# Optimization experiments

Measured on AMD Instinct MI355X. Metric: run time of the kernel, lower is better.

Reference implementation:

```python
import jax, jax.numpy as jnp
import numpy as np

H = 16         # num query heads
KV = 8         # num kv heads
HD = 64        # head_dim
WINDOW = 512   # sliding window size
ROPE_BASE = 10000.0


def rotate_half(x):
    x1, x2 = x[..., : x.shape[-1] // 2], x[..., x.shape[-1] // 2 :]
    return jnp.concatenate((-x2, x1), axis=-1)


def rope_cos_sin(seq_len, dim, dtype):
    inv_freq = 1.0 / (ROPE_BASE ** (jnp.arange(0, dim, 2, dtype=jnp.float32) / dim))
    t = jnp.arange(seq_len, dtype=jnp.float32)
    freqs = jnp.outer(t, inv_freq)              # [S, dim/2]
    emb = jnp.concatenate((freqs, freqs), axis=-1)  # [S, dim]
    return jnp.cos(emb).astype(dtype), jnp.sin(emb).astype(dtype)


def setup_inputs() -> dict:
    key = jax.random.key(0)
    ks = jax.random.split(key, 5)
    B, S, D = 2, 2048, 1024
    std = 0.02
    return {
        "hidden_states": jax.random.normal(ks[0], (B, S, D), dtype=jnp.float32),
        "Wq": jax.random.normal(ks[1], (D, H * HD), dtype=jnp.float32) * std,
        "Wk": jax.random.normal(ks[2], (D, KV * HD), dtype=jnp.float32) * std,
        "Wv": jax.random.normal(ks[3], (D, KV * HD), dtype=jnp.float32) * std,
        "Wo": jax.random.normal(ks[4], (H * HD, D), dtype=jnp.float32) * std,
    }


def reference(hidden_states, Wq, Wk, Wv, Wo):
    B, S, D = hidden_states.shape
    n_rep = H // KV

    q = (hidden_states @ Wq).reshape(B, S, H, HD).transpose(0, 2, 1, 3)   # [B,H,S,hd]
    k = (hidden_states @ Wk).reshape(B, S, KV, HD).transpose(0, 2, 1, 3)  # [B,KV,S,hd]
    v = (hidden_states @ Wv).reshape(B, S, KV, HD).transpose(0, 2, 1, 3)

    cos, sin = rope_cos_sin(S, HD, q.dtype)  # [S,hd]
    cos = cos[None, None]
    sin = sin[None, None]
    q = q * cos + rotate_half(q) * sin
    k = k * cos + rotate_half(k) * sin

    # repeat kv heads for GQA ([:, :, None] expand + reshape == repeat along head axis)
    k = jnp.repeat(k, n_rep, axis=1)  # [B,H,S,hd]
    v = jnp.repeat(v, n_rep, axis=1)

    scores = jnp.einsum("bhqd,bhkd->bhqk", q, k) / jnp.sqrt(jnp.asarray(HD, q.dtype))
    i = jnp.arange(S)[:, None]
    j = jnp.arange(S)[None, :]
    allowed = (j <= i) & (j >= i - WINDOW)  # causal + sliding window
    scores = jnp.where(allowed[None, None], scores, -jnp.inf)

    attn = jax.nn.softmax(scores, axis=-1)
    out = jnp.einsum("bhqk,bhkd->bhqd", attn, v)          # [B,H,S,hd]
    out = out.transpose(0, 2, 1, 3).reshape(B, S, H * HD)  # [B,S,D]
    return out @ Wo
```

## Files before the change

kernel.cpp:

```cpp
#include <hip/hip_runtime.h>
#include <hip/hip_bf16.h>

typedef __attribute__((ext_vector_type(8))) short short8;
typedef __attribute__((ext_vector_type(4))) float f32x4;

#define S_LEN 2048
#define NH 16
#define NKV 8
#define HD 64
#define WIN 512
#define DMODEL 1024
#define LOG2_10000 13.287712379549449f

#define GLOAD16(g, l)                                                        \
    __builtin_amdgcn_global_load_lds(                                        \
        (const __attribute__((address_space(1))) unsigned int*)(g),          \
        (__attribute__((address_space(3))) unsigned int*)(l), 16, 0, 0)

__device__ __forceinline__ int xcd_swz(int lin, int nwg) {
    return (lin & 7) * (nwg >> 3) + (lin >> 3);
}

__global__ void prep_kernel(const float* __restrict__ X,
                            const float* __restrict__ W0,
                            const float* __restrict__ W1,
                            const float* __restrict__ W2,
                            const float* __restrict__ W3,
                            __hip_bfloat16* __restrict__ Xb,
                            __hip_bfloat16* __restrict__ WqkvT,
                            __hip_bfloat16* __restrict__ WoT) {
    if (blockIdx.z == 4) {
        int tid = (blockIdx.y * 32 + blockIdx.x) * 256 + threadIdx.y * 32 + threadIdx.x;
        const float4* Xi = reinterpret_cast<const float4*>(X);
#pragma unroll
        for (int r = 0; r < 4; ++r) {
            int i = tid + r * (1024 * 256);
            float4 v = Xi[i];
            alignas(8) __hip_bfloat16 h[4];
            h[0] = __float2bfloat16(v.x);
            h[1] = __float2bfloat16(v.y);
            h[2] = __float2bfloat16(v.z);
            h[3] = __float2bfloat16(v.w);
            *reinterpret_cast<ushort4*>(Xb + (size_t)i * 4) =
                *reinterpret_cast<ushort4*>(h);
        }
        return;
    }
    __shared__ float tile[32][33];
    const int K = DMODEL;
    const float* W;
    __hip_bfloat16* WT;
    int N;
    switch (blockIdx.z) {
        case 0: W = W0; WT = WqkvT;                          N = 1024; break;
        case 1: W = W1; WT = WqkvT + (size_t)1024 * K;       N = 512;  break;
        case 2: W = W2; WT = WqkvT + (size_t)1536 * K;       N = 512;  break;
        default: W = W3; WT = WoT;                           N = 1024; break;
    }
    if ((int)blockIdx.x * 32 >= N) return;
    int nx = blockIdx.x * 32 + threadIdx.x;
    int k0 = blockIdx.y * 32;
#pragma unroll
    for (int r = 0; r < 4; ++r) {
        int k = k0 + threadIdx.y + r * 8;
        tile[threadIdx.y + r * 8][threadIdx.x] = W[(size_t)k * N + nx];
    }
    __syncthreads();
#pragma unroll
    for (int r = 0; r < 4; ++r) {
        int nn = blockIdx.x * 32 + threadIdx.y + r * 8;
        int kk = k0 + threadIdx.x;
        WT[(size_t)nn * K + kk] = __float2bfloat16(tile[threadIdx.x][threadIdx.y + r * 8]);
    }
}

__global__ __launch_bounds__(256, 2) void gemm_qkv_kernel(
    const __hip_bfloat16* __restrict__ A,
    const __hip_bfloat16* __restrict__ BT,
    __hip_bfloat16* __restrict__ Qo,
    __hip_bfloat16* __restrict__ Ko,
    __hip_bfloat16* __restrict__ VTo) {
    const int K = DMODEL;
    __shared__ __hip_bfloat16 ldsA[2][128 * 64];
    __shared__ __hip_bfloat16 ldsB[2][128 * 64];
    const int tx = threadIdx.x;
    const int wave = tx >> 6;
    const int lane = tx & 63;
    const int l16 = lane & 15;
    const int quad = lane >> 4;
    const int swz = xcd_swz(blockIdx.x + 16 * blockIdx.y, 512);
    const int col0 = (swz & 15) * 128;
    const int row0 = (swz >> 4) * 128;
    const int wrow = (wave >> 1) * 64;
    const int wcol = (wave & 1) * 64;
    const int sw = l16 & 7;

    f32x4 acc[4][4] = {};

    const int arow = tx >> 3;
    const int cs8 = ((tx & 7) ^ (arow & 7)) * 8;
    const __hip_bfloat16* gA = A + (size_t)(row0 + arow) * K + cs8;
    const __hip_bfloat16* gB = BT + (size_t)(col0 + arow) * K + cs8;

    auto stage = [&](int k0, int bf) {
        char* lA = (char*)(&ldsA[bf][0]) + tx * 16;
        char* lB = (char*)(&ldsB[bf][0]) + tx * 16;
#pragma unroll
        for (int r = 0; r < 4; ++r) {
            GLOAD16(gA + (size_t)(r * 32) * K + k0, lA + r * 4096);
            GLOAD16(gB + (size_t)(r * 32) * K + k0, lB + r * 4096);
        }
    };

    stage(0, 0);
    int buf = 0;
    for (int k0 = 0; k0 < K; k0 += 64) {
        __syncthreads();
        if (k0 + 64 < K) stage(k0 + 64, buf ^ 1);
        short8 af[4][2], bf4[4][2];
#pragma unroll
        for (int i = 0; i < 4; ++i) {
            const char* ar = (const char*)(&ldsA[buf][0]) + (wrow + i * 16 + l16) * 128;
            const char* br = (const char*)(&ldsB[buf][0]) + (wcol + i * 16 + l16) * 128;
#pragma unroll
            for (int ks = 0; ks < 2; ++ks) {
                af[i][ks] = *reinterpret_cast<const short8*>(
                    ar + (((ks * 4 + quad) ^ sw) << 4));
                bf4[i][ks] = *reinterpret_cast<const short8*>(
                    br + (((ks * 4 + quad) ^ sw) << 4));
            }
        }
#pragma unroll
        for (int ks = 0; ks < 2; ++ks)
#pragma unroll
            for (int mi = 0; mi < 4; ++mi)
#pragma unroll
                for (int ni = 0; ni < 4; ++ni)
                    acc[mi][ni] = __builtin_amdgcn_mfma_f32_16x16x32_bf16(
                        af[mi][ks], bf4[ni][ks], acc[mi][ni], 0, 0, 0);
        buf ^= 1;
    }

    const int rbase = row0 + wrow;
    const int cbaseg = col0 + wcol;
    const bool isQ = (cbaseg < DMODEL);
    const bool isK = (cbaseg >= DMODEL) && (cbaseg < DMODEL + 512);
    if (isQ || isK) {
        float invf[2];
        invf[0] = exp2f(-(float)(l16)      * (LOG2_10000 / 32.0f));
        invf[1] = exp2f(-(float)(16 + l16) * (LOG2_10000 / 32.0f));
#pragma unroll
        for (int mi = 0; mi < 4; ++mi)
#pragma unroll
            for (int r = 0; r < 4; ++r) {
                int srow = (rbase + mi * 16 + quad * 4 + r) & (S_LEN - 1);
#pragma unroll
                for (int ni = 0; ni < 2; ++ni) {
                    float ang = (float)srow * invf[ni];
                    float c = __cosf(ang), s = __sinf(ang);
                    float x1 = acc[mi][ni][r], x2 = acc[mi][ni + 2][r];
                    acc[mi][ni][r]     = x1 * c - x2 * s;
                    acc[mi][ni + 2][r] = x2 * c + x1 * s;
                }
            }
        __hip_bfloat16* Co = isQ ? Qo : Ko;
        int cbase = isQ ? cbaseg : cbaseg - DMODEL;
        int rowstride = isQ ? (NH * HD) : (NKV * HD);
#pragma unroll
        for (int mi = 0; mi < 4; ++mi)
#pragma unroll
            for (int ni = 0; ni < 4; ++ni) {
                size_t col = cbase + ni * 16 + l16;
#pragma unroll
                for (int r = 0; r < 4; ++r)
                    Co[(size_t)(rbase + mi * 16 + quad * 4 + r) * rowstride + col] =
                        __float2bfloat16(acc[mi][ni][r]);
            }
    } else {
        int bb = row0 >> 11;
#pragma unroll
        for (int mi = 0; mi < 4; ++mi) {
            int s = ((rbase + mi * 16 + quad * 4) & (S_LEN - 1));
#pragma unroll
            for (int ni = 0; ni < 4; ++ni) {
                int colv = cbaseg - 1536 + ni * 16 + l16;
                int vh = colv >> 6, d = colv & 63;
                alignas(8) __hip_bfloat16 hv[4];
#pragma unroll
                for (int r = 0; r < 4; ++r) hv[r] = __float2bfloat16(acc[mi][ni][r]);
                *reinterpret_cast<ushort4*>(
                    VTo + ((size_t)(bb * NKV + vh) * HD + d) * S_LEN + s) =
                    *reinterpret_cast<ushort4*>(hv);
            }
        }
    }
}

__global__ __launch_bounds__(256, 4) void gemm_op_kernel(
    const __hip_bfloat16* __restrict__ A,
    const __hip_bfloat16* __restrict__ BT,
    float* __restrict__ Co, int N, int K) {
    __shared__ __hip_bfloat16 ldsA[2][128 * 64];
    __shared__ __hip_bfloat16 ldsB[2][64 * 64];
    const int tx = threadIdx.x;
    const int wave = tx >> 6;
    const int lane = tx & 63;
    const int l16 = lane & 15;
    const int quad = lane >> 4;
    const int swz = xcd_swz(blockIdx.x + 16 * blockIdx.y, 512);
    const int col0 = (swz & 15) * 64;
    const int row0 = (swz >> 4) * 128;
    const int wrow = wave * 32;
    const int sw = l16 & 7;

    f32x4 acc[2][4] = {};

    const int arow = tx >> 3;
    const int cs8 = ((tx & 7) ^ (arow & 7)) * 8;
    const __hip_bfloat16* gA = A + (size_t)(row0 + arow) * K + cs8;
    const __hip_bfloat16* gB = BT + (size_t)(col0 + arow) * K + cs8;

    auto stage = [&](int k0, int bf) {
        char* lA = (char*)(&ldsA[bf][0]) + tx * 16;
        char* lB = (char*)(&ldsB[bf][0]) + tx * 16;
#pragma unroll
        for (int r = 0; r < 4; ++r)
            GLOAD16(gA + (size_t)(r * 32) * K + k0, lA + r * 4096);
#pragma unroll
        for (int r = 0; r < 2; ++r)
            GLOAD16(gB + (size_t)(r * 32) * K + k0, lB + r * 4096);
    };

    stage(0, 0);
    int buf = 0;
    for (int k0 = 0; k0 < K; k0 += 64) {
        __syncthreads();
        if (k0 + 64 < K) stage(k0 + 64, buf ^ 1);
        short8 af[2][2], bf4[4][2];
#pragma unroll
        for (int i = 0; i < 2; ++i) {
            const char* ar = (const char*)(&ldsA[buf][0]) + (wrow + i * 16 + l16) * 128;
#pragma unroll
            for (int ks = 0; ks < 2; ++ks)
                af[i][ks] = *reinterpret_cast<const short8*>(
                    ar + (((ks * 4 + quad) ^ sw) << 4));
        }
#pragma unroll
        for (int i = 0; i < 4; ++i) {
            const char* br = (const char*)(&ldsB[buf][0]) + (i * 16 + l16) * 128;
#pragma unroll
            for (int ks = 0; ks < 2; ++ks)
                bf4[i][ks] = *reinterpret_cast<const short8*>(
                    br + (((ks * 4 + quad) ^ sw) << 4));
        }
#pragma unroll
        for (int ks = 0; ks < 2; ++ks)
#pragma unroll
            for (int mi = 0; mi < 2; ++mi)
#pragma unroll
                for (int ni = 0; ni < 4; ++ni)
                    acc[mi][ni] = __builtin_amdgcn_mfma_f32_16x16x32_bf16(
                        af[mi][ks], bf4[ni][ks], acc[mi][ni], 0, 0, 0);
        buf ^= 1;
    }

    const int rbase = row0 + wrow;
#pragma unroll
    for (int mi = 0; mi < 2; ++mi)
#pragma unroll
        for (int ni = 0; ni < 4; ++ni) {
            size_t col = col0 + ni * 16 + l16;
#pragma unroll
            for (int r = 0; r < 4; ++r)
                Co[(size_t)(rbase + mi * 16 + quad * 4 + r) * N + col] = acc[mi][ni][r];
        }
}

__global__ __launch_bounds__(256, 4) void attn_mfma_kernel(
    const __hip_bfloat16* __restrict__ Q,
    const __hip_bfloat16* __restrict__ K,
    const __hip_bfloat16* __restrict__ VT,
    __hip_bfloat16* __restrict__ O) {
    __shared__ __hip_bfloat16 ldsK[2][64][64];
    __shared__ __hip_bfloat16 ldsVT[2][64][64];
    __shared__ __hip_bfloat16 ldsP[4][16][64];
    const int tx = threadIdx.x;
    const int wave = tx >> 6;
    const int lane = tx & 63;
    const int l16 = lane & 15;
    const int quad = lane >> 4;
    const int swz = xcd_swz(blockIdx.x + 32 * (blockIdx.y + 16 * blockIdx.z), 1024);
    const int q0 = (swz & 31) * 64;
    const int h = (swz >> 5) & 15;
    const int b = swz >> 9;
    const int kvh = h >> 1;
    const int qi = q0 + wave * 16 + l16;

    short8 aq[2];
    {
        const __hip_bfloat16* qp =
            Q + (size_t)(b * S_LEN + qi) * (NH * HD) + h * HD + quad * 8;
        aq[0] = *reinterpret_cast<const short8*>(qp);
        aq[1] = *reinterpret_cast<const short8*>(qp + 32);
    }
    f32x4 acc_o[4] = {};
    float m = -1e30f, l = 0.f;
    const float SL2 = 0.125f * 1.4426950408889634f;

    const int s_row = tx >> 3;
    const int s_c8 = (((tx & 7) ^ (s_row & 7))) * 8;
    const int sw = (l16 & 7);
    auto stage = [&](int j0, int bf) {
        char* lk = (char*)(&ldsK[bf][0][0]) + tx * 16;
        char* lv = (char*)(&ldsVT[bf][0][0]) + tx * 16;
#pragma unroll
        for (int r = 0; r < 2; ++r) {
            int row = s_row + r * 32;
            GLOAD16(K + (size_t)(b * S_LEN + j0 + row) * (NKV * HD) + kvh * HD + s_c8,
                    lk + r * 4096);
            GLOAD16(VT + ((size_t)(b * NKV + kvh) * HD + row) * S_LEN + j0 + s_c8,
                    lv + r * 4096);
        }
    };

    const int kstart = (q0 >= WIN) ? (q0 - WIN) : 0;
    stage(kstart, 0);
    int buf = 0;

    char* prow = (char*)(&ldsP[wave][l16][0]);

    for (int j0 = kstart; j0 <= q0; j0 += 64) {
        __syncthreads();
        if (j0 + 64 <= q0) stage(j0 + 64, buf ^ 1);

        f32x4 sacc[4] = {};
#pragma unroll
        for (int t = 0; t < 4; ++t) {
            const __hip_bfloat16* krow = &ldsK[buf][t * 16 + l16][0];
            short8 bk0 = *reinterpret_cast<const short8*>(krow + ((quad ^ sw) * 8));
            short8 bk1 = *reinterpret_cast<const short8*>(krow + (((4 + quad) ^ sw) * 8));
            sacc[t] = __builtin_amdgcn_mfma_f32_16x16x32_bf16(bk0, aq[0], sacc[t], 0, 0, 0);
            sacc[t] = __builtin_amdgcn_mfma_f32_16x16x32_bf16(bk1, aq[1], sacc[t], 0, 0, 0);
        }

        const bool need_mask = (j0 == q0) || (q0 >= WIN && j0 == kstart);
        float sv[4][4];
        if (need_mask) {
#pragma unroll
            for (int t = 0; t < 4; ++t)
#pragma unroll
                for (int r = 0; r < 4; ++r) {
                    int j = j0 + t * 16 + quad * 4 + r;
                    bool ok = (j <= qi) && (j + WIN >= qi);
                    sv[t][r] = ok ? sacc[t][r] * SL2 : -1e30f;
                }
        } else {
#pragma unroll
            for (int t = 0; t < 4; ++t)
#pragma unroll
                for (int r = 0; r < 4; ++r) sv[t][r] = sacc[t][r] * SL2;
        }
        float cm = -1e30f;
#pragma unroll
        for (int t = 0; t < 4; ++t)
#pragma unroll
            for (int r = 0; r < 4; ++r) cm = fmaxf(cm, sv[t][r]);
        cm = fmaxf(cm, __shfl_xor(cm, 16));
        cm = fmaxf(cm, __shfl_xor(cm, 32));
        if (!__all(cm - m <= 8.0f)) {
            float mn = fmaxf(m, cm);
            float alpha = exp2f(m - mn);
            m = mn;
            l *= alpha;
#pragma unroll
            for (int t = 0; t < 4; ++t)
#pragma unroll
                for (int r = 0; r < 4; ++r) acc_o[t][r] *= alpha;
        }
        float sp = 0.f;
#pragma unroll
        for (int t = 0; t < 4; ++t)
#pragma unroll
            for (int r = 0; r < 4; ++r) { sv[t][r] = exp2f(sv[t][r] - m); sp += sv[t][r]; }
        sp += __shfl_xor(sp, 16);
        sp += __shfl_xor(sp, 32);
        l += sp;
#pragma unroll
        for (int t = 0; t < 4; ++t) {
            alignas(8) __hip_bfloat16 hp[4];
#pragma unroll
            for (int r = 0; r < 4; ++r) hp[r] = __float2bfloat16(sv[t][r]);
            int swb = ((((2 * t + (quad >> 1)) ^ (l16 & 7)) << 4) | ((quad & 1) << 3));
            *reinterpret_cast<ushort4*>(prow + swb) = *reinterpret_cast<ushort4*>(hp);
        }

#pragma unroll
        for (int ks = 0; ks < 2; ++ks) {
            short8 pf = *reinterpret_cast<const short8*>(
                prow + (((4 * ks + quad) ^ (l16 & 7)) << 4));
#pragma unroll
            for (int t = 0; t < 4; ++t) {
                const __hip_bfloat16* vrow = &ldsVT[buf][t * 16 + l16][0];
                short8 vf = *reinterpret_cast<const short8*>(
                    vrow + (((ks * 4 + quad) ^ sw) * 8));
                acc_o[t] = __builtin_amdgcn_mfma_f32_16x16x32_bf16(vf, pf, acc_o[t], 0, 0, 0);
            }
        }
        buf ^= 1;
    }

    {
        float inv = 1.f / l;
        __hip_bfloat16* op =
            O + (size_t)(b * S_LEN + qi) * (NH * HD) + h * HD;
#pragma unroll
        for (int t = 0; t < 4; ++t) {
            alignas(8) __hip_bfloat16 ho[4];
#pragma unroll
            for (int r = 0; r < 4; ++r) ho[r] = __float2bfloat16(acc_o[t][r] * inv);
            *reinterpret_cast<ushort4*>(op + t * 16 + quad * 4) =
                *reinterpret_cast<ushort4*>(ho);
        }
    }
}

extern "C" void kernel_launch(void* const* d_in, const int* in_sizes, int n_in,
                              void* d_out, int out_size, void* d_ws, size_t ws_size,
                              hipStream_t stream) {
    const float* X  = (const float*)d_in[0];
    const float* Wq = (const float*)d_in[1];
    const float* Wk = (const float*)d_in[2];
    const float* Wv = (const float*)d_in[3];
    const float* Wo = (const float*)d_in[4];
    float* out = (float*)d_out;

    const int ROWS = 2 * S_LEN;
    char* ws = (char*)d_ws;
    size_t off = 0;
    __hip_bfloat16* Xb     = (__hip_bfloat16*)(ws + off); off += (size_t)ROWS * DMODEL * 2;
    __hip_bfloat16* WqkvT  = (__hip_bfloat16*)(ws + off); off += (size_t)2048 * DMODEL * 2;
    __hip_bfloat16* WoT    = (__hip_bfloat16*)(ws + off); off += (size_t)DMODEL * DMODEL * 2;
    __hip_bfloat16* Qb     = (__hip_bfloat16*)(ws + off); off += (size_t)ROWS * (NH * HD) * 2;
    __hip_bfloat16* Kb     = (__hip_bfloat16*)(ws + off); off += (size_t)ROWS * (NKV * HD) * 2;
    __hip_bfloat16* VTg    = (__hip_bfloat16*)(ws + off); off += (size_t)ROWS * (NKV * HD) * 2;
    __hip_bfloat16* Ob     = (__hip_bfloat16*)(ws + off); off += (size_t)ROWS * (NH * HD) * 2;

    prep_kernel<<<dim3(32, 32, 5), dim3(32, 8), 0, stream>>>(
        X, Wq, Wk, Wv, Wo, Xb, WqkvT, WoT);

    gemm_qkv_kernel<<<dim3(2048 / 128, ROWS / 128), 256, 0, stream>>>(
        Xb, WqkvT, Qb, Kb, VTg);

    attn_mfma_kernel<<<dim3(S_LEN / 64, NH, 2), 256, 0, stream>>>(Qb, Kb, VTg, Ob);

    gemm_op_kernel<<<dim3(DMODEL / 64, ROWS / 128), 256, 0, stream>>>(
        Ob, WoT, out, DMODEL, DMODEL);
}
```

Measured before the change: 146.3 us.

## Load K and V tiles directly from global memory instead of staging through LDS

The attention kernel stops double-buffering K and V^T tiles in shared memory with async global-to-LDS loads and block-wide barriers. Each wave now reads its MFMA operands for K and V straight from global memory, relying on L1/L2 caching. This removes the per-iteration __syncthreads and the LDS footprint, which may raise occupancy. The cost is that the four waves each fetch the same K/V data redundantly, with no software prefetch to hide global latency.

```diff
diff --git a/kernel.cpp b/kernel.cpp
--- a/kernel.cpp
+++ b/kernel.cpp
@@ -281,8 +281,6 @@
     const __hip_bfloat16* __restrict__ K,
     const __hip_bfloat16* __restrict__ VT,
     __hip_bfloat16* __restrict__ O) {
-    __shared__ __hip_bfloat16 ldsK[2][64][64];
-    __shared__ __hip_bfloat16 ldsVT[2][64][64];
     __shared__ __hip_bfloat16 ldsP[4][16][64];
     const int tx = threadIdx.x;
     const int wave = tx >> 6;
@@ -307,38 +305,22 @@
     float m = -1e30f, l = 0.f;
     const float SL2 = 0.125f * 1.4426950408889634f;
 
-    const int s_row = tx >> 3;
-    const int s_c8 = (((tx & 7) ^ (s_row & 7))) * 8;
-    const int sw = (l16 & 7);
-    auto stage = [&](int j0, int bf) {
-        char* lk = (char*)(&ldsK[bf][0][0]) + tx * 16;
-        char* lv = (char*)(&ldsVT[bf][0][0]) + tx * 16;
-#pragma unroll
-        for (int r = 0; r < 2; ++r) {
-            int row = s_row + r * 32;
-            GLOAD16(K + (size_t)(b * S_LEN + j0 + row) * (NKV * HD) + kvh * HD + s_c8,
-                    lk + r * 4096);
-            GLOAD16(VT + ((size_t)(b * NKV + kvh) * HD + row) * S_LEN + j0 + s_c8,
-                    lv + r * 4096);
-        }
-    };
+    const __hip_bfloat16* Kbase =
+        K + (size_t)b * S_LEN * (NKV * HD) + kvh * HD + quad * 8;
+    const __hip_bfloat16* Vbase =
+        VT + ((size_t)(b * NKV + kvh) * HD + l16) * S_LEN;
 
     const int kstart = (q0 >= WIN) ? (q0 - WIN) : 0;
-    stage(kstart, 0);
-    int buf = 0;
-
     char* prow = (char*)(&ldsP[wave][l16][0]);
 
     for (int j0 = kstart; j0 <= q0; j0 += 64) {
-        __syncthreads();
-        if (j0 + 64 <= q0) stage(j0 + 64, buf ^ 1);
-
         f32x4 sacc[4] = {};
 #pragma unroll
         for (int t = 0; t < 4; ++t) {
-            const __hip_bfloat16* krow = &ldsK[buf][t * 16 + l16][0];
-            short8 bk0 = *reinterpret_cast<const short8*>(krow + ((quad ^ sw) * 8));
-            short8 bk1 = *reinterpret_cast<const short8*>(krow + (((4 + quad) ^ sw) * 8));
+            const __hip_bfloat16* krow =
+                Kbase + (size_t)(j0 + t * 16 + l16) * (NKV * HD);
+            short8 bk0 = *reinterpret_cast<const short8*>(krow);
+            short8 bk1 = *reinterpret_cast<const short8*>(krow + 32);
             sacc[t] = __builtin_amdgcn_mfma_f32_16x16x32_bf16(bk0, aq[0], sacc[t], 0, 0, 0);
             sacc[t] = __builtin_amdgcn_mfma_f32_16x16x32_bf16(bk1, aq[1], sacc[t], 0, 0, 0);
         }
@@ -400,13 +382,12 @@
                 prow + (((4 * ks + quad) ^ (l16 & 7)) << 4));
 #pragma unroll
             for (int t = 0; t < 4; ++t) {
-                const __hip_bfloat16* vrow = &ldsVT[buf][t * 16 + l16][0];
-                short8 vf = *reinterpret_cast<const short8*>(
-                    vrow + (((ks * 4 + quad) ^ sw) * 8));
+                const __hip_bfloat16* vrow =
+                    Vbase + (size_t)(t * 16) * S_LEN + j0 + (ks * 4 + quad) * 8;
+                short8 vf = *reinterpret_cast<const short8*>(vrow);
                 acc_o[t] = __builtin_amdgcn_mfma_f32_16x16x32_bf16(vf, pf, acc_o[t], 0, 0, 0);
             }
         }
-        buf ^= 1;
     }
 
     {
```

After: 187.5 us. 28.1% more time.
